# Kernel optimization log

Hardware: AMD Instinct MI355X
Metric: run time of the kernel (lower is better)

Reference implementation:

```python
import jax, jax.numpy as jnp
import numpy as np

B, H, S, Dh = 2, 16, 2048, 64


def setup_inputs() -> dict:
    key = jax.random.key(0)
    kq, kk, kv = jax.random.split(key, 3)
    query = jax.random.normal(kq, (B, H, S, Dh), dtype=jnp.float32)
    k = jax.random.normal(kk, (B, H, S, Dh), dtype=jnp.float32)
    value = jax.random.normal(kv, (B, H, S, Dh), dtype=jnp.float32)
    mask = jnp.zeros((1, 1, S, S), dtype=jnp.float32)
    return {"query": query, "key": k, "value": value, "mask": mask}


def reference(query, key, value, mask):
    # scores: [B,H,S,S]
    dk = jnp.asarray(key.shape[-1], dtype=query.dtype)
    logits = jnp.einsum("bhqd,bhkd->bhqk", query, key) / jnp.sqrt(dk)
    logits = logits + mask * (-1e9)
    attention_weights = jax.nn.softmax(logits, axis=-1)
    output = jnp.einsum("bhqk,bhkd->bhqd", attention_weights, value)
    return (output, attention_weights)
```

## Files before the change

kernel.cpp:

```cpp
#include <hip/hip_runtime.h>
#include <hip/hip_bf16.h>
#include <stdint.h>

typedef __bf16 bf16;
typedef __attribute__((ext_vector_type(8))) __bf16 bf16x8;
typedef __attribute__((ext_vector_type(4))) float f32x4;

constexpr int S   = 2048;
constexpr int DH  = 64;
constexpr int BQ  = 16;
constexpr int NW  = 4;
constexpr int KPW = S / NW;
constexpr int NC  = KPW / 32;
constexpr int BH  = 32;
constexpr size_t ELEMS = (size_t)BH * S * DH;
constexpr size_t WS_NEED = ELEMS * 2 * 3;


__global__ __launch_bounds__(256)
void cast_kq(const float* __restrict__ K, const float* __restrict__ Q,
             bf16* __restrict__ Kb, bf16* __restrict__ Qb)
{
    const size_t t = (size_t)blockIdx.x * 256 + threadIdx.x;
    {
        const float* src = K + t * 8;
        f32x4 a = *(const f32x4*)(src);
        f32x4 b = *(const f32x4*)(src + 4);
        bf16x8 o;
        #pragma unroll
        for (int j = 0; j < 4; ++j) { o[j] = (bf16)a[j]; o[j + 4] = (bf16)b[j]; }
        *(bf16x8*)(Kb + t * 8) = o;
    }
    {
        const float* src = Q + t * 8;
        f32x4 a = *(const f32x4*)(src);
        f32x4 b = *(const f32x4*)(src + 4);
        bf16x8 o;
        #pragma unroll
        for (int j = 0; j < 4; ++j) { o[j] = (bf16)a[j]; o[j + 4] = (bf16)b[j]; }
        *(bf16x8*)(Qb + t * 8) = o;
    }
}

__global__ __launch_bounds__(256)
void transpose_v(const float* __restrict__ V, bf16* __restrict__ Vt)
{
    __shared__ bf16 t[64][72];
    const int bh = blockIdx.x >> 5;
    const int sb = (blockIdx.x & 31) * 64;
    const int tid = threadIdx.x;

    {
        const int r  = tid >> 2;
        const int c0 = (tid & 3) * 16;
        const float* src = V + ((size_t)bh * S + sb + r) * DH + c0;
        f32x4 v0 = *(const f32x4*)(src);
        f32x4 v1 = *(const f32x4*)(src + 4);
        f32x4 v2 = *(const f32x4*)(src + 8);
        f32x4 v3 = *(const f32x4*)(src + 12);
        #pragma unroll
        for (int j = 0; j < 4; ++j) {
            t[r][c0 + j]      = (bf16)v0[j];
            t[r][c0 + 4 + j]  = (bf16)v1[j];
            t[r][c0 + 8 + j]  = (bf16)v2[j];
            t[r][c0 + 12 + j] = (bf16)v3[j];
        }
    }
    __syncthreads();
    {
        const int d  = tid >> 2;
        const int s0 = (tid & 3) * 16;
        bf16x8 o0, o1;
        #pragma unroll
        for (int j = 0; j < 8; ++j) { o0[j] = t[s0 + j][d]; o1[j] = t[s0 + 8 + j][d]; }
        bf16* dst = Vt + ((size_t)bh * DH + d) * S + sb + s0;
        *(bf16x8*)(dst)     = o0;
        *(bf16x8*)(dst + 8) = o1;
    }
}

__global__ __launch_bounds__(256)
void attn_fused_b16(const bf16* __restrict__ Qb, const bf16* __restrict__ Kb,
                    const bf16* __restrict__ Vt, const float* __restrict__ Msk,
                    float* __restrict__ Out, float* __restrict__ W)
{
    __shared__ float rs[NW][BQ];
    __shared__ float inv[BQ];
    __shared__ float opart[NW][BQ][DH];

    const int tid  = threadIdx.x;
    const int lane = tid & 63;
    const int wave = tid >> 6;
    const int c    = lane & 15;
    const int g    = lane >> 4;

    const int swz = (blockIdx.x & 7) * 512 + (blockIdx.x >> 3);
    const int bh = swz >> 7;
    const int q0 = (swz & 127) * BQ;

    const bf16* Qbb = Qb + (size_t)bh * S * DH;
    const bf16* Kbb = Kb + (size_t)bh * S * DH;
    const bf16* Vtb = Vt + (size_t)bh * DH * S;

    const bf16* qr = Qbb + (size_t)(q0 + c) * DH + g * 8;
    bf16x8 qlo = *(const bf16x8*)(qr);
    bf16x8 qhi = *(const bf16x8*)(qr + 32);

    const int kbase = wave * KPW;
    const int cperm = 8 * (c >> 2) + (c & 3);
    const float* mrow = Msk + (size_t)(q0 + c) * S;

    bf16x8 pa[NC];
    float s = 0.f;
    #pragma unroll
    for (int kc = 0; kc < NC; ++kc) {
        const int k0 = kbase + kc * 32;
        const bf16* kr = Kbb + (size_t)(k0 + cperm) * DH + g * 8;
        bf16x8 kl0 = *(const bf16x8*)(kr);
        bf16x8 kh0 = *(const bf16x8*)(kr + 32);
        bf16x8 kl1 = *(const bf16x8*)(kr + 4 * DH);
        bf16x8 kh1 = *(const bf16x8*)(kr + 4 * DH + 32);
        f32x4 m0 = *(const f32x4*)(mrow + k0 + 8 * g);
        f32x4 m1 = *(const f32x4*)(mrow + k0 + 8 * g + 4);

        f32x4 acc0 = {0.f, 0.f, 0.f, 0.f};
        f32x4 acc1 = {0.f, 0.f, 0.f, 0.f};
        acc0 = __builtin_amdgcn_mfma_f32_16x16x32_bf16(kl0, qlo, acc0, 0, 0, 0);
        acc0 = __builtin_amdgcn_mfma_f32_16x16x32_bf16(kh0, qhi, acc0, 0, 0, 0);
        acc1 = __builtin_amdgcn_mfma_f32_16x16x32_bf16(kl1, qlo, acc1, 0, 0, 0);
        acc1 = __builtin_amdgcn_mfma_f32_16x16x32_bf16(kh1, qhi, acc1, 0, 0, 0);

        #pragma unroll
        for (int r = 0; r < 4; ++r) {
            const float p0 = __expf(acc0[r] * 0.125f + m0[r] * (-1e9f));
            const float p1 = __expf(acc1[r] * 0.125f + m1[r] * (-1e9f));
            s += p0 + p1;
            pa[kc][r]     = (bf16)p0;
            pa[kc][r + 4] = (bf16)p1;
        }
    }

    s += __shfl_xor(s, 16);
    s += __shfl_xor(s, 32);
    if (lane < 16) rs[wave][lane] = s;
    __syncthreads();
    if (tid < BQ) {
        float t = 0.f;
        #pragma unroll
        for (int w = 0; w < NW; ++w) t += rs[w][tid];
        inv[tid] = 1.f / t;
    }
    __syncthreads();
    const float myinv = inv[c];

    f32x4 oacc[4] = {{0,0,0,0},{0,0,0,0},{0,0,0,0},{0,0,0,0}};
    float* Wrow = W + (size_t)bh * S * S + (size_t)(q0 + c) * S;

    #pragma unroll
    for (int kc = 0; kc < NC; ++kc) {
        const int k0 = kbase + kc * 32;

        const bf16* vp = Vtb + (size_t)c * S + k0 + 8 * g;
        bf16x8 vb0 = *(const bf16x8*)(vp);
        bf16x8 vb1 = *(const bf16x8*)(vp + (size_t)16 * S);
        bf16x8 vb2 = *(const bf16x8*)(vp + (size_t)32 * S);
        bf16x8 vb3 = *(const bf16x8*)(vp + (size_t)48 * S);

        f32x4 w0, w1;
        #pragma unroll
        for (int r = 0; r < 4; ++r) {
            w0[r] = (float)pa[kc][r]     * myinv;
            w1[r] = (float)pa[kc][r + 4] * myinv;
        }
        *(f32x4*)(Wrow + k0 + 8 * g)     = w0;
        *(f32x4*)(Wrow + k0 + 8 * g + 4) = w1;

        oacc[0] = __builtin_amdgcn_mfma_f32_16x16x32_bf16(pa[kc], vb0, oacc[0], 0, 0, 0);
        oacc[1] = __builtin_amdgcn_mfma_f32_16x16x32_bf16(pa[kc], vb1, oacc[1], 0, 0, 0);
        oacc[2] = __builtin_amdgcn_mfma_f32_16x16x32_bf16(pa[kc], vb2, oacc[2], 0, 0, 0);
        oacc[3] = __builtin_amdgcn_mfma_f32_16x16x32_bf16(pa[kc], vb3, oacc[3], 0, 0, 0);
    }

    #pragma unroll
    for (int dt = 0; dt < 4; ++dt)
        #pragma unroll
        for (int r = 0; r < 4; ++r)
            opart[wave][4 * g + r][16 * dt + c] = oacc[dt][r];
    __syncthreads();

    {
        const int q = tid >> 4;
        const int d = (tid & 15) * 4;
        f32x4 o = {0.f, 0.f, 0.f, 0.f};
        #pragma unroll
        for (int w = 0; w < NW; ++w) o += *(const f32x4*)&opart[w][q][d];
        const float is = inv[q];
        o.x *= is; o.y *= is; o.z *= is; o.w *= is;
        float* Ob = Out + ((size_t)bh * S + q0 + q) * DH + d;
        *(f32x4*)Ob = o;
    }
}

__global__ __launch_bounds__(256)
void attn_fused_f32(const float* __restrict__ Q, const float* __restrict__ K,
                    const float* __restrict__ V, const float* __restrict__ Msk,
                    float* __restrict__ Out, float* __restrict__ W)
{
    __shared__ float rs[NW][BQ];
    __shared__ float inv[BQ];
    __shared__ float opart[NW][BQ][DH];

    const int tid  = threadIdx.x;
    const int lane = tid & 63;
    const int wave = tid >> 6;
    const int c    = lane & 15;
    const int g    = lane >> 4;

    const int swz = (blockIdx.x & 7) * 512 + (blockIdx.x >> 3);
    const int bh = swz >> 7;
    const int q0 = (swz & 127) * BQ;

    const float* Qb = Q + (size_t)bh * S * DH;
    const float* Kb = K + (size_t)bh * S * DH;
    const float* Vb = V + (size_t)bh * S * DH;

    bf16x8 qlo, qhi;
    {
        const float* qr = Qb + (size_t)(q0 + c) * DH + g * 8;
        f32x4 a0 = *(const f32x4*)(qr);
        f32x4 a1 = *(const f32x4*)(qr + 4);
        f32x4 b0 = *(const f32x4*)(qr + 32);
        f32x4 b1 = *(const f32x4*)(qr + 36);
        #pragma unroll
        for (int j = 0; j < 4; ++j) {
            qlo[j]     = (bf16)a0[j];  qlo[j + 4] = (bf16)a1[j];
            qhi[j]     = (bf16)b0[j];  qhi[j + 4] = (bf16)b1[j];
        }
    }

    const int kbase = wave * KPW;
    const int cperm = 8 * (c >> 2) + (c & 3);
    const float* mrow = Msk + (size_t)(q0 + c) * S;

    bf16x8 pa[NC];
    float s = 0.f;
    #pragma unroll
    for (int kc = 0; kc < NC; ++kc) {
        const int k0 = kbase + kc * 32;
        const float* kr0 = Kb + (size_t)(k0 + cperm) * DH + g * 8;
        const float* kr1 = kr0 + (size_t)4 * DH;
        f32x4 a0 = *(const f32x4*)(kr0);
        f32x4 a1 = *(const f32x4*)(kr0 + 4);
        f32x4 b0 = *(const f32x4*)(kr0 + 32);
        f32x4 b1 = *(const f32x4*)(kr0 + 36);
        f32x4 a2 = *(const f32x4*)(kr1);
        f32x4 a3 = *(const f32x4*)(kr1 + 4);
        f32x4 b2 = *(const f32x4*)(kr1 + 32);
        f32x4 b3 = *(const f32x4*)(kr1 + 36);
        f32x4 m0 = *(const f32x4*)(mrow + k0 + 8 * g);
        f32x4 m1 = *(const f32x4*)(mrow + k0 + 8 * g + 4);

        bf16x8 kl0, kh0, kl1, kh1;
        #pragma unroll
        for (int j = 0; j < 4; ++j) {
            kl0[j] = (bf16)a0[j];  kl0[j + 4] = (bf16)a1[j];
            kh0[j] = (bf16)b0[j];  kh0[j + 4] = (bf16)b1[j];
            kl1[j] = (bf16)a2[j];  kl1[j + 4] = (bf16)a3[j];
            kh1[j] = (bf16)b2[j];  kh1[j + 4] = (bf16)b3[j];
        }
        f32x4 acc0 = {0.f, 0.f, 0.f, 0.f};
        f32x4 acc1 = {0.f, 0.f, 0.f, 0.f};
        acc0 = __builtin_amdgcn_mfma_f32_16x16x32_bf16(kl0, qlo, acc0, 0, 0, 0);
        acc0 = __builtin_amdgcn_mfma_f32_16x16x32_bf16(kh0, qhi, acc0, 0, 0, 0);
        acc1 = __builtin_amdgcn_mfma_f32_16x16x32_bf16(kl1, qlo, acc1, 0, 0, 0);
        acc1 = __builtin_amdgcn_mfma_f32_16x16x32_bf16(kh1, qhi, acc1, 0, 0, 0);

        #pragma unroll
        for (int r = 0; r < 4; ++r) {
            const float p0 = __expf(acc0[r] * 0.125f + m0[r] * (-1e9f));
            const float p1 = __expf(acc1[r] * 0.125f + m1[r] * (-1e9f));
            s += p0 + p1;
            pa[kc][r]     = (bf16)p0;
            pa[kc][r + 4] = (bf16)p1;
        }
    }

    s += __shfl_xor(s, 16);
    s += __shfl_xor(s, 32);
    if (lane < 16) rs[wave][lane] = s;
    __syncthreads();
    if (tid < BQ) {
        float t = 0.f;
        #pragma unroll
        for (int w = 0; w < NW; ++w) t += rs[w][tid];
        inv[tid] = 1.f / t;
    }
    __syncthreads();
    const float myinv = inv[c];

    f32x4 oacc[4] = {{0,0,0,0},{0,0,0,0},{0,0,0,0},{0,0,0,0}};
    float* Wrow = W + (size_t)bh * S * S + (size_t)(q0 + c) * S;

    #pragma unroll
    for (int kc = 0; kc < NC; ++kc) {
        const int k0 = kbase + kc * 32;
        const float* vp = Vb + (size_t)(k0 + 8 * g) * DH + c;
        float vv[4][8];
        #pragma unroll
        for (int j = 0; j < 8; ++j) {
            #pragma unroll
            for (int dt = 0; dt < 4; ++dt)
                vv[dt][j] = vp[j * DH + dt * 16];
        }
        f32x4 w0, w1;
        #pragma unroll
        for (int r = 0; r < 4; ++r) {
            w0[r] = (float)pa[kc][r]     * myinv;
            w1[r] = (float)pa[kc][r + 4] * myinv;
        }
        *(f32x4*)(Wrow + k0 + 8 * g)     = w0;
        *(f32x4*)(Wrow + k0 + 8 * g + 4) = w1;

        #pragma unroll
        for (int dt = 0; dt < 4; ++dt) {
            bf16x8 vb;
            #pragma unroll
            for (int j = 0; j < 8; ++j) vb[j] = (bf16)vv[dt][j];
            oacc[dt] = __builtin_amdgcn_mfma_f32_16x16x32_bf16(pa[kc], vb, oacc[dt], 0, 0, 0);
        }
    }

    #pragma unroll
    for (int dt = 0; dt < 4; ++dt)
        #pragma unroll
        for (int r = 0; r < 4; ++r)
            opart[wave][4 * g + r][16 * dt + c] = oacc[dt][r];
    __syncthreads();

    {
        const int q = tid >> 4;
        const int d = (tid & 15) * 4;
        f32x4 o = {0.f, 0.f, 0.f, 0.f};
        #pragma unroll
        for (int w = 0; w < NW; ++w) o += *(const f32x4*)&opart[w][q][d];
        const float is = inv[q];
        o.x *= is; o.y *= is; o.z *= is; o.w *= is;
        float* Ob = Out + ((size_t)bh * S + q0 + q) * DH + d;
        *(f32x4*)Ob = o;
    }
}

extern "C" void kernel_launch(void* const* d_in, const int* in_sizes, int n_in,
                              void* d_out, int out_size, void* d_ws, size_t ws_size,
                              hipStream_t stream) {
    const float* Q   = (const float*)d_in[0];
    const float* K   = (const float*)d_in[1];
    const float* V   = (const float*)d_in[2];
    const float* Msk = (const float*)d_in[3];

    float* Out = (float*)d_out;
    float* W   = Out + (size_t)2 * 16 * 2048 * 64;

    if (ws_size >= WS_NEED) {
        bf16* Kb = (bf16*)d_ws;
        bf16* Vt = Kb + ELEMS;
        bf16* Qb = Vt + ELEMS;
        hipLaunchKernelGGL(cast_kq, dim3(ELEMS / 8 / 256), dim3(256), 0, stream,
                           K, Q, Kb, Qb);
        hipLaunchKernelGGL(transpose_v, dim3(BH * (S / 64)), dim3(256), 0, stream,
                           V, Vt);
        hipLaunchKernelGGL(attn_fused_b16, dim3(BH * (S / BQ)), dim3(256), 0, stream,
                           Qb, Kb, Vt, Msk, Out, W);
    } else {
        hipLaunchKernelGGL(attn_fused_f32, dim3(BH * (S / BQ)), dim3(256), 0, stream,
                           Q, K, V, Msk, Out, W);
    }
}
```

Measured before the change: 366.2 us.

## Widen attention block to 16 waves and pre-scale mask to bf16

The main attention kernel now runs 1024 threads (16 waves) per 16-query block, so each wave covers 128 keys instead of 512. This lowers per-wave register use for the probability buffer and adds parallelism per block. A new prep kernel converts the mask into bf16 already multiplied by -1e9, halving mask read traffic in the main kernel, at the cost of an extra launch and a bf16 rounding of the mask bias. Cross-wave reduction through shared memory grows with 16 partial outputs.

```diff
diff --git a/kernel.cpp b/kernel.cpp
--- a/kernel.cpp
+++ b/kernel.cpp
@@ -9,12 +9,13 @@
 constexpr int S   = 2048;
 constexpr int DH  = 64;
 constexpr int BQ  = 16;
-constexpr int NW  = 4;
+constexpr int BH  = 32;
+constexpr int NW  = 16;
 constexpr int KPW = S / NW;
 constexpr int NC  = KPW / 32;
-constexpr int BH  = 32;
-constexpr size_t ELEMS = (size_t)BH * S * DH;
-constexpr size_t WS_NEED = ELEMS * 2 * 3;
+constexpr size_t ELEMS   = (size_t)BH * S * DH;
+constexpr size_t WS_QKV  = ELEMS * 2 * 3;
+constexpr size_t WS_FULL = WS_QKV + (size_t)S * S * 2;
 
 
 __global__ __launch_bounds__(256)
@@ -80,9 +81,27 @@
 }
 
 __global__ __launch_bounds__(256)
-void attn_fused_b16(const bf16* __restrict__ Qb, const bf16* __restrict__ Kb,
-                    const bf16* __restrict__ Vt, const float* __restrict__ Msk,
-                    float* __restrict__ Out, float* __restrict__ W)
+void prep_mask(const float* __restrict__ M, bf16* __restrict__ Mb)
+{
+    const size_t t = (size_t)blockIdx.x * 256 + threadIdx.x;
+    const float* src = M + t * 8;
+    f32x4 a = *(const f32x4*)(src);
+    f32x4 b = *(const f32x4*)(src + 4);
+    bf16x8 o;
+    #pragma unroll
+    for (int j = 0; j < 4; ++j) {
+        o[j]     = (bf16)(a[j] * -1e9f);
+        o[j + 4] = (bf16)(b[j] * -1e9f);
+    }
+    *(bf16x8*)(Mb + t * 8) = o;
+}
+
+template<bool MB16>
+__global__ __launch_bounds__(1024)
+void attn_main(const bf16* __restrict__ Qb, const bf16* __restrict__ Kb,
+               const bf16* __restrict__ Vt, const bf16* __restrict__ Mb,
+               const float* __restrict__ Mf,
+               float* __restrict__ Out, float* __restrict__ W)
 {
     __shared__ float rs[NW][BQ];
     __shared__ float inv[BQ];
@@ -108,7 +127,8 @@
 
     const int kbase = wave * KPW;
     const int cperm = 8 * (c >> 2) + (c & 3);
-    const float* mrow = Msk + (size_t)(q0 + c) * S;
+    const bf16*  mrow16 = MB16 ? (Mb + (size_t)(q0 + c) * S) : nullptr;
+    const float* mrowf  = MB16 ? nullptr : (Mf + (size_t)(q0 + c) * S);
 
     bf16x8 pa[NC];
     float s = 0.f;
@@ -120,8 +140,18 @@
         bf16x8 kh0 = *(const bf16x8*)(kr + 32);
         bf16x8 kl1 = *(const bf16x8*)(kr + 4 * DH);
         bf16x8 kh1 = *(const bf16x8*)(kr + 4 * DH + 32);
-        f32x4 m0 = *(const f32x4*)(mrow + k0 + 8 * g);
-        f32x4 m1 = *(const f32x4*)(mrow + k0 + 8 * g + 4);
+
+        float mv[8];
+        if constexpr (MB16) {
+            bf16x8 mm = *(const bf16x8*)(mrow16 + k0 + 8 * g);
+            #pragma unroll
+            for (int j = 0; j < 8; ++j) mv[j] = (float)mm[j];
+        } else {
+            f32x4 a = *(const f32x4*)(mrowf + k0 + 8 * g);
+            f32x4 b = *(const f32x4*)(mrowf + k0 + 8 * g + 4);
+            #pragma unroll
+            for (int j = 0; j < 4; ++j) { mv[j] = a[j] * -1e9f; mv[j + 4] = b[j] * -1e9f; }
+        }
 
         f32x4 acc0 = {0.f, 0.f, 0.f, 0.f};
         f32x4 acc1 = {0.f, 0.f, 0.f, 0.f};
@@ -132,8 +162,8 @@
 
         #pragma unroll
         for (int r = 0; r < 4; ++r) {
-            const float p0 = __expf(acc0[r] * 0.125f + m0[r] * (-1e9f));
-            const float p1 = __expf(acc1[r] * 0.125f + m1[r] * (-1e9f));
+            const float p0 = __expf(acc0[r] * 0.125f + mv[r]);
+            const float p1 = __expf(acc1[r] * 0.125f + mv[r + 4]);
             s += p0 + p1;
             pa[kc][r]     = (bf16)p0;
             pa[kc][r + 4] = (bf16)p1;
@@ -188,7 +218,7 @@
             opart[wave][4 * g + r][16 * dt + c] = oacc[dt][r];
     __syncthreads();
 
-    {
+    if (tid < BQ * 16) {
         const int q = tid >> 4;
         const int d = (tid & 15) * 4;
         f32x4 o = {0.f, 0.f, 0.f, 0.f};
@@ -201,14 +231,18 @@
     }
 }
 
+constexpr int NWF  = 4;
+constexpr int KPWF = S / NWF;
+constexpr int NCF  = KPWF / 32;
+
 __global__ __launch_bounds__(256)
 void attn_fused_f32(const float* __restrict__ Q, const float* __restrict__ K,
                     const float* __restrict__ V, const float* __restrict__ Msk,
                     float* __restrict__ Out, float* __restrict__ W)
 {
-    __shared__ float rs[NW][BQ];
+    __shared__ float rs[NWF][BQ];
     __shared__ float inv[BQ];
-    __shared__ float opart[NW][BQ][DH];
+    __shared__ float opart[NWF][BQ][DH];
 
     const int tid  = threadIdx.x;
     const int lane = tid & 63;
@@ -238,14 +272,14 @@
         }
     }
 
-    const int kbase = wave * KPW;
+    const int kbase = wave * KPWF;
     const int cperm = 8 * (c >> 2) + (c & 3);
     const float* mrow = Msk + (size_t)(q0 + c) * S;
 
-    bf16x8 pa[NC];
+    bf16x8 pa[NCF];
     float s = 0.f;
     #pragma unroll
-    for (int kc = 0; kc < NC; ++kc) {
+    for (int kc = 0; kc < NCF; ++kc) {
         const int k0 = kbase + kc * 32;
         const float* kr0 = Kb + (size_t)(k0 + cperm) * DH + g * 8;
         const float* kr1 = kr0 + (size_t)4 * DH;
@@ -292,7 +326,7 @@
     if (tid < BQ) {
         float t = 0.f;
         #pragma unroll
-        for (int w = 0; w < NW; ++w) t += rs[w][tid];
+        for (int w = 0; w < NWF; ++w) t += rs[w][tid];
         inv[tid] = 1.f / t;
     }
     __syncthreads();
@@ -302,7 +336,7 @@
     float* Wrow = W + (size_t)bh * S * S + (size_t)(q0 + c) * S;
 
     #pragma unroll
-    for (int kc = 0; kc < NC; ++kc) {
+    for (int kc = 0; kc < NCF; ++kc) {
         const int k0 = kbase + kc * 32;
         const float* vp = Vb + (size_t)(k0 + 8 * g) * DH + c;
         float vv[4][8];
@@ -342,7 +376,7 @@
         const int d = (tid & 15) * 4;
         f32x4 o = {0.f, 0.f, 0.f, 0.f};
         #pragma unroll
-        for (int w = 0; w < NW; ++w) o += *(const f32x4*)&opart[w][q][d];
+        for (int w = 0; w < NWF; ++w) o += *(const f32x4*)&opart[w][q][d];
         const float is = inv[q];
         o.x *= is; o.y *= is; o.z *= is; o.w *= is;
         float* Ob = Out + ((size_t)bh * S + q0 + q) * DH + d;
@@ -361,7 +395,9 @@
     float* Out = (float*)d_out;
     float* W   = Out + (size_t)2 * 16 * 2048 * 64;
 
-    if (ws_size >= WS_NEED) {
+    const dim3 gmain(BH * (S / BQ));
+
+    if (ws_size >= WS_QKV) {
         bf16* Kb = (bf16*)d_ws;
         bf16* Vt = Kb + ELEMS;
         bf16* Qb = Vt + ELEMS;
@@ -369,10 +405,18 @@
                            K, Q, Kb, Qb);
         hipLaunchKernelGGL(transpose_v, dim3(BH * (S / 64)), dim3(256), 0, stream,
                            V, Vt);
-        hipLaunchKernelGGL(attn_fused_b16, dim3(BH * (S / BQ)), dim3(256), 0, stream,
-                           Qb, Kb, Vt, Msk, Out, W);
+        if (ws_size >= WS_FULL) {
+            bf16* Mb = Qb + ELEMS;
+            hipLaunchKernelGGL(prep_mask, dim3((S * (size_t)S) / 8 / 256), dim3(256),
+                               0, stream, Msk, Mb);
+            hipLaunchKernelGGL((attn_main<true>), gmain, dim3(1024), 0, stream,
+                               Qb, Kb, Vt, Mb, nullptr, Out, W);
+        } else {
+            hipLaunchKernelGGL((attn_main<false>), gmain, dim3(1024), 0, stream,
+                               Qb, Kb, Vt, nullptr, Msk, Out, W);
+        }
     } else {
-        hipLaunchKernelGGL(attn_fused_f32, dim3(BH * (S / BQ)), dim3(256), 0, stream,
+        hipLaunchKernelGGL(attn_fused_f32, gmain, dim3(256), 0, stream,
                            Q, K, V, Msk, Out, W);
     }
 }
```

Result: slower. 378.7 us (+3.4%).
